# Kernel tuning notes

Hardware: AMD Instinct MI355X
Metric: run time of the kernel (lower is better)

Reference implementation:

```python
import jax, jax.numpy as jnp
import numpy as np
import jax.scipy.linalg as jsl


def _rbf(X1, X2, log_lengthscale):
    # squared-exponential kernel: exp(-0.5 * ||x1 - x2||^2 / ls^2)
    ls2 = jnp.exp(2.0 * log_lengthscale)
    d2 = (jnp.sum(X1 * X1, axis=1)[:, None]
          + jnp.sum(X2 * X2, axis=1)[None, :]
          - 2.0 * (X1 @ X2.T))
    return jnp.exp(-0.5 * jnp.maximum(d2, 0.0) / ls2)


def setup_inputs() -> dict:
    key = jax.random.key(0)
    k1, k2, k3, k4, k5 = jax.random.split(key, 5)
    N, D, l, rank, N_ = 1024, 8, 4, 2, 1024
    return {
        "X": jax.random.normal(k1, (N, D), dtype=jnp.float32),
        "test_X": jax.random.normal(k2, (N_, D), dtype=jnp.float32),
        "Y": jax.random.normal(k3, (N, l), dtype=jnp.float32),
        "log_noise": jnp.zeros((l,), dtype=jnp.float32),
        "covar_factor": jax.random.normal(k4, (l, rank), dtype=jnp.float32),
        "log_var": jax.random.normal(k5, (l,), dtype=jnp.float32),
        "log_lengthscale": jnp.zeros((), dtype=jnp.float32),
    }


def reference(X, test_X, Y, log_noise, covar_factor, log_var, log_lengthscale):
    N, l = Y.shape
    N_ = test_X.shape[0]
    # IndexKernel: B B^T + diag(exp(log_var))   -> (l, l)
    task_K = covar_factor @ covar_factor.T + jnp.diag(jnp.exp(log_var))
    # per-task noise kron identity -> (N*l, N*l)
    noise = jnp.kron(jnp.diag(jnp.exp(log_noise)), jnp.eye(N, dtype=X.dtype))
    # full Kronecker covariance and its Cholesky factor
    K = jnp.kron(task_K, _rbf(X, X, log_lengthscale)) + noise
    L = jnp.linalg.cholesky(K)                       # (N*l, N*l), lower
    Kx = jnp.kron(task_K, _rbf(X, test_X, log_lengthscale))     # (N*l, N_*l)
    Kxx = jnp.kron(task_K, _rbf(test_X, test_X, log_lengthscale))  # (N_*l, N_*l)
    A = jsl.solve_triangular(L, Kx, lower=True)      # L A = Kx
    Y_vec = Y.T.reshape(-1, 1)                        # vec of Y^T, (N*l, 1)
    V = jsl.solve_triangular(L, Y_vec, lower=True)
    fmean = A.T @ V                                   # (N_*l, 1)
    fvar = Kxx - A.T @ A                              # (N_*l, N_*l)
    return fmean, fvar, noise, fmean.reshape(l, N_).T
```

## Files before the change

### kernel.cpp

```cpp
#include <hip/hip_runtime.h>
#include <math.h>

#define NN 1024
#define NM (NN*NN)
#define NB 64
#define NBLK 16
#define NW 1152
#define BIG 4096

#define OFF_FVAR  ((size_t)4096)
#define OFF_NOISE ((size_t)(4096 + 16777216))
#define OFF_M4    ((size_t)(4096 + 2*16777216))

#define CPAD(c) ((c) + (((c)>>5)<<2))
#define WSTRIDE 140

struct GPParams {
  float tk[16];
  float E[16];
  float G[16];
  float lam[4];
};

__global__ void k_prep(const float* __restrict__ logn, const float* __restrict__ cf,
                       const float* __restrict__ logv, GPParams* __restrict__ P)
{
  if (threadIdx.x != 0 || blockIdx.x != 0) return;
  double tk[4][4], Dn[4], T[4][4], U[4][4];
  for (int a=0;a<4;a++) for (int b=0;b<4;b++){
    double s = 0.0;
    for (int r=0;r<2;r++) s += (double)cf[a*2+r]*(double)cf[b*2+r];
    if (a==b) s += exp((double)logv[a]);
    tk[a][b] = s;
  }
  for (int a=0;a<4;a++) Dn[a] = exp((double)logn[a]);
  for (int a=0;a<4;a++) for (int b=0;b<4;b++)
    T[a][b] = tk[a][b]/sqrt(Dn[a]*Dn[b]);
  for (int a=0;a<4;a++) for (int b=0;b<4;b++) U[a][b] = (a==b)?1.0:0.0;
  for (int sweep=0; sweep<40; sweep++){
    for (int p=0;p<3;p++) for (int q=p+1;q<4;q++){
      double apq = T[p][q];
      if (fabs(apq) < 1e-300) continue;
      double tau = (T[q][q]-T[p][p])/(2.0*apq);
      double t = (tau >= 0.0) ? 1.0/(tau + sqrt(1.0+tau*tau))
                              : 1.0/(tau - sqrt(1.0+tau*tau));
      double c = 1.0/sqrt(1.0+t*t), s = t*c;
      for (int k=0;k<4;k++){ double akp=T[k][p], akq=T[k][q];
        T[k][p]=c*akp - s*akq; T[k][q]=s*akp + c*akq; }
      for (int k=0;k<4;k++){ double apk=T[p][k], aqk=T[q][k];
        T[p][k]=c*apk - s*aqk; T[q][k]=s*apk + c*aqk; }
      for (int k=0;k<4;k++){ double ukp=U[k][p], ukq=U[k][q];
        U[k][p]=c*ukp - s*ukq; U[k][q]=s*ukp + c*ukq; }
    }
  }
  double E[4][4], G[4][4];
  for (int a=0;a<4;a++) for (int i=0;i<4;i++) E[a][i] = U[a][i]/sqrt(Dn[a]);
  for (int a=0;a<4;a++) for (int i=0;i<4;i++){
    double s=0; for (int b=0;b<4;b++) s += tk[a][b]*E[b][i];
    G[a][i]=s;
  }
  for (int a=0;a<4;a++) for (int b=0;b<4;b++){
    P->tk[a*4+b] = (float)tk[a][b];
    P->E [a*4+b] = (float)E[a][b];
    P->G [a*4+b] = (float)G[a][b];
  }
  for (int i=0;i<4;i++){
    double l = T[i][i];
    P->lam[i] = (float)(l > 0.0 ? l : 0.0);
  }
}

__global__ void k_rbf(const float* __restrict__ X1, const float* __restrict__ X2,
                      const float* __restrict__ logls, float* __restrict__ out)
{
  __shared__ float x1s[16][8];
  __shared__ float x2s[16][8];
  int tx = threadIdx.x, ty = threadIdx.y;
  int tid = ty*16 + tx;
  if (tid < 128){
    int r = tid>>3, d = tid&7;
    x1s[r][d] = X1[((size_t)blockIdx.y*16 + r)*8 + d];
  } else {
    int t2 = tid-128, r = t2>>3, d = t2&7;
    x2s[r][d] = X2[((size_t)blockIdx.x*16 + r)*8 + d];
  }
  __syncthreads();
  float ls2 = expf(2.0f*logls[0]);
  float d2 = 0.f;
  #pragma unroll
  for (int d=0; d<8; d++){ float df = x1s[ty][d]-x2s[tx][d]; d2 += df*df; }
  int i = blockIdx.y*16+ty, j = blockIdx.x*16+tx;
  out[(size_t)i*NN + j] = expf(-0.5f*d2/ls2);
}

__global__ void k_rbfM(const float* __restrict__ X1, const float* __restrict__ logls,
                       const GPParams* __restrict__ P, float* __restrict__ M)
{
  __shared__ float x1s[16][8];
  __shared__ float x2s[16][8];
  int tx = threadIdx.x, ty = threadIdx.y;
  int tid = ty*16 + tx;
  if (tid < 128){
    int r = tid>>3, d = tid&7;
    x1s[r][d] = X1[((size_t)blockIdx.y*16 + r)*8 + d];
  } else {
    int t2 = tid-128, r = t2>>3, d = t2&7;
    x2s[r][d] = X1[((size_t)blockIdx.x*16 + r)*8 + d];
  }
  __syncthreads();
  float ls2 = expf(2.0f*logls[0]);
  float d2 = 0.f;
  #pragma unroll
  for (int d=0; d<8; d++){ float df = x1s[ty][d]-x2s[tx][d]; d2 += df*df; }
  int i = blockIdx.y*16+ty, j = blockIdx.x*16+tx;
  float v = expf(-0.5f*d2/ls2);
  float diag = (i==j) ? 1.f : 0.f;
  size_t idx = (size_t)i*NN + j;
  #pragma unroll
  for (int z=0;z<4;z++)
    M[(size_t)z*NM + idx] = P->lam[z]*v + diag;
}

__global__ void k_uvec(const float* __restrict__ Y, const GPParams* __restrict__ P,
                       float* __restrict__ u)
{
  int n = blockIdx.x*256 + threadIdx.x;
  float y0 = Y[n*4+0], y1 = Y[n*4+1], y2 = Y[n*4+2], y3 = Y[n*4+3];
  #pragma unroll
  for (int i=0;i<4;i++)
    u[i*NN + n] = P->E[0*4+i]*y0 + P->E[1*4+i]*y1 + P->E[2*4+i]*y2 + P->E[3*4+i]*y3;
}

__device__ __forceinline__ void gemm64(const float* __restrict__ A, const float* __restrict__ B,
                                       float acc[4][4], int r0, int c0, bool sub)
{
  for (int p=0;p<64;p++){
    float ar[4], bc[4];
    #pragma unroll
    for (int ii=0;ii<4;ii++) ar[ii]=A[(r0+ii)*65+p];
    #pragma unroll
    for (int jj=0;jj<4;jj++) bc[jj]=B[p*65+c0+jj];
    if (sub){
      #pragma unroll
      for (int ii=0;ii<4;ii++)
        #pragma unroll
        for (int jj=0;jj<4;jj++) acc[ii][jj] -= ar[ii]*bc[jj];
    } else {
      #pragma unroll
      for (int ii=0;ii<4;ii++)
        #pragma unroll
        for (int jj=0;jj<4;jj++) acc[ii][jj] += ar[ii]*bc[jj];
    }
  }
}
__device__ __forceinline__ void gemm64T(const float* __restrict__ A, const float* __restrict__ B,
                                        float acc[4][4], int r0, int c0)
{
  for (int p=0;p<64;p++){
    float ar[4], bc[4];
    #pragma unroll
    for (int ii=0;ii<4;ii++) ar[ii]=A[(r0+ii)*65+p];
    #pragma unroll
    for (int jj=0;jj<4;jj++) bc[jj]=B[(c0+jj)*65+p];
    #pragma unroll
    for (int ii=0;ii<4;ii++)
      #pragma unroll
      for (int jj=0;jj<4;jj++) acc[ii][jj] += ar[ii]*bc[jj];
  }
}

__device__ __forceinline__ void inv_lower64(const float* __restrict__ L,
                                            float* __restrict__ inv,
                                            float* __restrict__ tmp, int tid)
{
  for (int idx=tid; idx<4160; idx+=256) inv[idx]=0.f;
  __syncthreads();
  if (tid < 64){
    int b = tid>>3, c = tid&7, base=b*8;
    for (int r=c;r<8;r++){
      float s = (r==c)?1.f:0.f;
      for (int j=c;j<r;j++) s -= L[(base+r)*65 + base+j]*inv[(base+j)*65 + base+c];
      inv[(base+r)*65 + base+c] = s / L[(base+r)*65 + base+r];
    }
  }
  __syncthreads();
  for (int bs=8; bs<=32; bs<<=1){
    int npair = 32/bs;
    int nout = npair*bs*bs;
    for (int idx=tid; idx<nout; idx+=256){
      int p0 = idx/(bs*bs), rem = idx%(bs*bs);
      int r = rem/bs, c = rem%bs, base = p0*2*bs;
      float s=0.f;
      for (int j=c;j<bs;j++)
        s += L[(base+bs+r)*65 + base+j]*inv[(base+j)*65 + base+c];
      tmp[idx]=s;
    }
    __syncthreads();
    for (int idx=tid; idx<nout; idx+=256){
      int p0 = idx/(bs*bs), rem = idx%(bs*bs);
      int r = rem/bs, c = rem%bs, base = p0*2*bs;
      float s=0.f;
      for (int j=0;j<=r;j++)
        s += inv[(base+bs+r)*65 + base+bs+j]*tmp[p0*bs*bs + j*bs + c];
      inv[(base+bs+r)*65 + base+c] = -s;
    }
    __syncthreads();
  }
}

__global__ __launch_bounds__(256) void k_potf2(float* __restrict__ M, float* __restrict__ Linv,
                                               float* __restrict__ Gbuf, int k)
{
  int z = blockIdx.x, tid = threadIdx.x;
  __shared__ float a[64*65];
  __shared__ float lo[64*65];
  __shared__ float tmp[1024];
  float* Mz = M + (size_t)z*NM;
  int base = k*NB;
  for (int idx=tid; idx<4096; idx+=256){
    int r=idx>>6, c=idx&63;
    a[r*65+c] = Mz[(size_t)(base+r)*NN + base + c];
  }
  int r = tid & 63, q = tid >> 6;
  for (int j=0;j<64;j++){
    __syncthreads();
    float d = a[j*65+j];
    float invd = 1.f/d;
    float rs = rsqrtf(d);
    if (q==0){
      if (r == j) lo[j*65+j] = sqrtf(d);
      else if (r > j) lo[r*65+j] = a[r*65+j]*rs;
      else lo[r*65+j] = 0.f;
    }
    if (r > j){
      float lrj = a[r*65+j]*invd;
      for (int c=j+1+q; c<=r; c+=4)
        a[r*65+c] -= lrj * a[c*65+j];
    }
  }
  __syncthreads();
  inv_lower64(lo, a, tmp, tid);
  float* Lg = Linv + ((size_t)z*NBLK + k)*(NB*NB);
  float* Td = Mz + (size_t)base*NN + base;
  for (int idx=tid; idx<4096; idx+=256){
    int rr=idx>>6, c=idx&63;
    float v = a[rr*65+c];
    Lg[rr*64+c] = v;
    Td[(size_t)rr*NN + c] = v;
  }
  {
    int r0=(tid>>4)*4, c0=(tid&15)*4;
    float g[4][4]={};
    for (int p=0;p<64;p++){
      float ar[4], bc[4];
      #pragma unroll
      for (int ii=0;ii<4;ii++) ar[ii]=a[p*65+r0+ii];
      #pragma unroll
      for (int jj=0;jj<4;jj++) bc[jj]=a[p*65+c0+jj];
      #pragma unroll
      for (int ii=0;ii<4;ii++)
        #pragma unroll
        for (int jj=0;jj<4;jj++) g[ii][jj]+=ar[ii]*bc[jj];
    }
    float* Gg = Gbuf + ((size_t)z*NBLK + k)*4096;
    #pragma unroll
    for (int ii=0;ii<4;ii++)
      *(float4*)&Gg[(r0+ii)*64 + c0] = make_float4(g[ii][0],g[ii][1],g[ii][2],g[ii][3]);
  }
}

__global__ __launch_bounds__(256) void k_csf(float* __restrict__ M, float* __restrict__ Linv,
                                             float* __restrict__ Gbuf, float* __restrict__ Lbuf, int k)
{
  int z = blockIdx.z;
  int tt = blockIdx.x, i2 = 0;
  while (tt >= i2+1){ tt -= (i2+1); i2++; }
  int bi = k+1+i2, bj = k+1+tt;
  bool fblk = (i2==0);
  __shared__ float pa[64*65];
  __shared__ float pb[64*65];
  __shared__ float li[64*65];
  float* Mz = M + (size_t)z*NM;
  float* Lb = Lbuf + (size_t)z*NM;
  int tid = threadIdx.x;
  int ty = tid>>4, tx = tid&15;
  int r0 = ty*4, c0 = tx*4;

  if (fblk){
    const float* Lg = Linv + ((size_t)z*NBLK + k)*(NB*NB);
    for (int idx=tid; idx<4096; idx+=256){
      int r=idx>>6, c=idx&63;
      li[r*65+c] = Lg[idx];
      pa[r*65+c] = Mz[(size_t)(bi*64+r)*NN + k*64 + c];
      pb[r*65+c] = Mz[(size_t)(bi*64+r)*NN + bi*64 + c];
    }
    __syncthreads();
    float sc[4][4]={};
    gemm64T(pa, li, sc, r0, c0);
    #pragma unroll
    for (int ii=0;ii<4;ii++)
      *(float4*)&Lb[(size_t)(bi*64+r0+ii)*NN + k*64+c0] =
        make_float4(sc[ii][0],sc[ii][1],sc[ii][2],sc[ii][3]);
    __syncthreads();
    #pragma unroll
    for (int ii=0;ii<4;ii++)
      #pragma unroll
      for (int jj=0;jj<4;jj++) pa[(r0+ii)*65+c0+jj] = sc[ii][jj];
    __syncthreads();
    float upd[4][4]={};
    gemm64T(pa, pa, upd, r0, c0);
    #pragma unroll
    for (int ii=0;ii<4;ii++)
      #pragma unroll
      for (int jj=0;jj<4;jj++) pb[(r0+ii)*65+c0+jj] -= upd[ii][jj];
    int r = tid & 63, q = tid >> 6;
    for (int j=0;j<64;j++){
      __syncthreads();
      float d = pb[j*65+j];
      float invd = 1.f/d;
      float rs = rsqrtf(d);
      if (q==0){
        if (r == j) li[j*65+j] = sqrtf(d);
        else if (r > j) li[r*65+j] = pb[r*65+j]*rs;
        else li[r*65+j] = 0.f;
      }
      if (r > j){
        float lrj = pb[r*65+j]*invd;
        for (int c=j+1+q; c<=r; c+=4)
          pb[r*65+c] -= lrj * pb[c*65+j];
      }
    }
    __syncthreads();
    inv_lower64(li, pa, pb, tid);
    float* Lg2 = Linv + ((size_t)z*NBLK + (k+1))*(NB*NB);
    float* Td  = Mz + (size_t)(bi*64)*NN + bi*64;
    for (int idx=tid; idx<4096; idx+=256){
      int rr=idx>>6, c=idx&63;
      float v = pa[rr*65+c];
      Lg2[rr*64+c] = v;
      Td[(size_t)rr*NN + c] = v;
    }
    {
      float g[4][4]={};
      for (int p=0;p<64;p++){
        float ar[4], bc[4];
        #pragma unroll
        for (int ii=0;ii<4;ii++) ar[ii]=pa[p*65+r0+ii];
        #pragma unroll
        for (int jj=0;jj<4;jj++) bc[jj]=pa[p*65+c0+jj];
        #pragma unroll
        for (int ii=0;ii<4;ii++)
          #pragma unroll
          for (int jj=0;jj<4;jj++) g[ii][jj]+=ar[ii]*bc[jj];
      }
      float* Gg = Gbuf + ((size_t)z*NBLK + (k+1))*4096;
      #pragma unroll
      for (int ii=0;ii<4;ii++)
        *(float4*)&Gg[(r0+ii)*64 + c0] = make_float4(g[ii][0],g[ii][1],g[ii][2],g[ii][3]);
    }
    return;
  }

  const float* Gg = Gbuf + ((size_t)z*NBLK + k)*4096;
  for (int idx=tid; idx<4096; idx+=256){
    int r=idx>>6, c=idx&63;
    li[r*65+c] = Gg[idx];
    pa[r*65+c] = Mz[(size_t)(bi*64+r)*NN + k*64 + c];
    pb[r*65+c] = Mz[(size_t)(bj*64+r)*NN + k*64 + c];
  }
  __syncthreads();
  float t[4][4]={};
  gemm64(pa, li, t, r0, c0, false);
  __syncthreads();
  #pragma unroll
  for (int ii=0;ii<4;ii++)
    #pragma unroll
    for (int jj=0;jj<4;jj++) li[(r0+ii)*65+c0+jj] = t[ii][jj];
  __syncthreads();
  float upd[4][4]={};
  gemm64T(li, pb, upd, r0, c0);
  #pragma unroll
  for (int ii=0;ii<4;ii++){
    float4* ptr = (float4*)&Mz[(size_t)(bi*64+r0+ii)*NN + bj*64+c0];
    float4 v = *ptr;
    v.x-=upd[ii][0]; v.y-=upd[ii][1]; v.z-=upd[ii][2]; v.w-=upd[ii][3];
    *ptr = v;
  }
  if (bj == k+1){
    __syncthreads();
    const float* Lg = Linv + ((size_t)z*NBLK + k)*(NB*NB);
    for (int idx=tid; idx<4096; idx+=256){
      int r=idx>>6, c=idx&63;
      pb[r*65+c] = Lg[idx];
    }
    __syncthreads();
    float sc[4][4]={};
    gemm64T(pa, pb, sc, r0, c0);
    #pragma unroll
    for (int ii=0;ii<4;ii++)
      *(float4*)&Lb[(size_t)(bi*64+r0+ii)*NN + k*64+c0] =
        make_float4(sc[ii][0],sc[ii][1],sc[ii][2],sc[ii][3]);
  }
}

__global__ __launch_bounds__(256) void k_dbl1(const float* __restrict__ Lbuf,
                                              const float* __restrict__ Linv,
                                              float* __restrict__ Tinv)
{
  int pair = blockIdx.x, z = blockIdx.y, tid = threadIdx.x;
  int b0 = 2*pair, b1 = 2*pair+1;
  __shared__ float l21[64*65];
  __shared__ float ai[64*65];
  __shared__ float tt[64*65];
  const float* Lb = Lbuf + (size_t)z*NM;
  const float* La = Linv + ((size_t)z*NBLK + b0)*(NB*NB);
  const float* Lc = Linv + ((size_t)z*NBLK + b1)*(NB*NB);
  for (int idx=tid; idx<4096; idx+=256){
    int r=idx>>6, c=idx&63;
    l21[r*65+c] = Lb[(size_t)(b1*64+r)*NN + b0*64 + c];
    ai[r*65+c]  = La[idx];
  }
  __syncthreads();
  int ty=tid>>4, tx=tid&15, r0=ty*4, c0=tx*4;
  float acc[4][4]={};
  gemm64(l21, ai, acc, r0, c0, false);
  __syncthreads();
  #pragma unroll
  for (int ii=0;ii<4;ii++)
    #pragma unroll
    for (int jj=0;jj<4;jj++) tt[(r0+ii)*65 + c0+jj] = acc[ii][jj];
  for (int idx=tid; idx<4096; idx+=256){
    int r=idx>>6, c=idx&63;
    ai[r*65+c] = Lc[idx];
  }
  __syncthreads();
  float fin[4][4]={};
  gemm64(ai, tt, fin, r0, c0, false);
  float* Tz = Tinv + (size_t)z*NM;
  #pragma unroll
  for (int ii=0;ii<4;ii++){
    float4 v = make_float4(-fin[ii][0],-fin[ii][1],-fin[ii][2],-fin[ii][3]);
    *(float4*)&Tz[(size_t)(b1*64+r0+ii)*NN + b0*64+c0] = v;
  }
}

__global__ __launch_bounds__(256) void k_dblT(const float* __restrict__ Lbuf,
                                              const float* __restrict__ Tinv,
                                              float* __restrict__ tb, int g64)
{
  int z = blockIdx.y, tid = threadIdx.x;
  int tpp = g64*g64;
  int pair = blockIdx.x / tpp;
  int tt2 = blockIdx.x % tpp;
  int ti = tt2 / g64, tj = tt2 % g64;
  int b0 = 2*pair*g64, b1 = b0 + g64;
  const float* Lb = Lbuf + (size_t)z*NM;
  const float* Tz = Tinv + (size_t)z*NM;
  __shared__ float lt[64*65];
  __shared__ float rt[64*65];
  int ty=tid>>4, tx=tid&15, r0=ty*4, c0=tx*4;
  float acc[4][4]={};
  for (int kb=tj; kb<g64; kb++){
    for (int idx=tid; idx<4096; idx+=256){
      int r=idx>>6, c=idx&63;
      lt[r*65+c] = Lb[(size_t)((b1+ti)*64+r)*NN + (b0+kb)*64 + c];
      rt[r*65+c] = Tz[(size_t)((b0+kb)*64+r)*NN + (b0+tj)*64 + c];
    }
    __syncthreads();
    gemm64(lt, rt, acc, r0, c0, false);
    __syncthreads();
  }
  int g = g64*64;
  float* tz = tb + (size_t)z*262144 + (size_t)pair*g*g;
  #pragma unroll
  for (int ii=0;ii<4;ii++){
    float4 v = make_float4(acc[ii][0],acc[ii][1],acc[ii][2],acc[ii][3]);
    *(float4*)&tz[(size_t)(ti*64+r0+ii)*g + tj*64+c0] = v;
  }
}

__global__ __launch_bounds__(256) void k_dblC(const float* __restrict__ tb,
                                              float* __restrict__ Tinv, int g64)
{
  int z = blockIdx.y, tid = threadIdx.x;
  int tpp = g64*g64;
  int pair = blockIdx.x / tpp;
  int tt2 = blockIdx.x % tpp;
  int ti = tt2 / g64, tj = tt2 % g64;
  int b0 = 2*pair*g64, b1 = b0 + g64;
  float* Tz = Tinv + (size_t)z*NM;
  int g = g64*64;
  const float* tz = tb + (size_t)z*262144 + (size_t)pair*g*g;
  __shared__ float lt[64*65];
  __shared__ float rt[64*65];
  int ty=tid>>4, tx=tid&15, r0=ty*4, c0=tx*4;
  float acc[4][4]={};
  for (int kb=0; kb<=ti; kb++){
    for (int idx=tid; idx<4096; idx+=256){
      int r=idx>>6, c=idx&63;
      lt[r*65+c] = Tz[(size_t)((b1+ti)*64+r)*NN + (b1+kb)*64 + c];
      rt[r*65+c] = tz[(size_t)(kb*64+r)*g + tj*64 + c];
    }
    __syncthreads();
    gemm64(lt, rt, acc, r0, c0, false);
    __syncthreads();
  }
  #pragma unroll
  for (int ii=0;ii<4;ii++){
    float4 v = make_float4(-acc[ii][0],-acc[ii][1],-acc[ii][2],-acc[ii][3]);
    *(float4*)&Tz[(size_t)((b1+ti)*64+r0+ii)*NN + b0*64+tj*64+c0] = v;
  }
}

__global__ __launch_bounds__(256) void k_wgemm(const float* __restrict__ Tinv,
                                               const float* __restrict__ R,
                                               const float* __restrict__ u,
                                               float* __restrict__ W)
{
  int ct = blockIdx.x;
  int bi = blockIdx.y;
  int z  = blockIdx.z;
  const float* Tz = Tinv + (size_t)z*NM;
  float* Wz = W + (size_t)z*NN*NW;
  __shared__ float At[64*68];
  __shared__ float Bs[64*132];
  int tid = threadIdx.x;
  int ty = tid>>4, tx = tid&15;
  float areg[16], breg[32];
  float acc[4][8] = {};
  #pragma unroll
  for (int i=0;i<16;i++){
    int idx=i*256+tid, r=idx>>6, c=idx&63;
    areg[i] = Tz[(size_t)(bi*64+r)*NN + c];
  }
  #pragma unroll
  for (int i=0;i<32;i++){
    int idx=i*256+tid, r=idx>>7, c=idx&127;
    breg[i] = (ct<8) ? R[(size_t)r*NN + ct*128 + c]
                     : ((c<4) ? u[c*NN + r] : 0.f);
  }
  for (int kb=0; kb<=bi; kb++){
    __syncthreads();
    #pragma unroll
    for (int i=0;i<16;i++){
      int idx=i*256+tid, r=idx>>6, c=idx&63;
      At[c*68 + r] = areg[i];
    }
    #pragma unroll
    for (int i=0;i<32;i++){
      int idx=i*256+tid, r=idx>>7, c=idx&127;
      Bs[r*132 + c] = breg[i];
    }
    if (kb < bi){
      int kn = kb+1;
      #pragma unroll
      for (int i=0;i<16;i++){
        int idx=i*256+tid, r=idx>>6, c=idx&63;
        areg[i] = Tz[(size_t)(bi*64+r)*NN + kn*64 + c];
      }
      #pragma unroll
      for (int i=0;i<32;i++){
        int idx=i*256+tid, r=idx>>7, c=idx&127;
        int gr = kn*64 + r;
        breg[i] = (ct<8) ? R[(size_t)gr*NN + ct*128 + c]
                         : ((c<4) ? u[c*NN + gr] : 0.f);
      }
    }
    __syncthreads();
    for (int p=0;p<64;p++){
      float4 a4 = *(const float4*)&At[p*68 + ty*4];
      float4 b0 = *(const float4*)&Bs[p*132 + tx*8];
      float4 b1 = *(const float4*)&Bs[p*132 + tx*8 + 4];
      float ar[4]={a4.x,a4.y,a4.z,a4.w};
      float bc[8]={b0.x,b0.y,b0.z,b0.w,b1.x,b1.y,b1.z,b1.w};
      #pragma unroll
      for (int ii=0;ii<4;ii++)
        #pragma unroll
        for (int jj=0;jj<8;jj++) acc[ii][jj] += ar[ii]*bc[jj];
    }
  }
  #pragma unroll
  for (int ii=0;ii<4;ii++){
    size_t row = (size_t)(bi*64 + ty*4 + ii)*NW + ct*128 + tx*8;
    *(float4*)&Wz[row]   = make_float4(acc[ii][0],acc[ii][1],acc[ii][2],acc[ii][3]);
    *(float4*)&Wz[row+4] = make_float4(acc[ii][4],acc[ii][5],acc[ii][6],acc[ii][7]);
  }
}

__global__ __launch_bounds__(256) void k_WtW(const float* __restrict__ W,
                                             float* __restrict__ Qa, float* __restrict__ Qb)
{
  int z = blockIdx.z;
  int ks = blockIdx.x / 36;
  int tt = blockIdx.x % 36, mi = 0;
  while (tt >= mi+1){ tt -= (mi+1); mi++; }
  int mj = tt;
  const float* Wz = W + (size_t)z*NN*NW;
  float* Qz = (ks ? Qb : Qa) + (size_t)z*NM;
  int mi0 = mi*128, mj0 = mj*128;
  __shared__ float as[16*WSTRIDE];
  __shared__ float bs[16*WSTRIDE];
  int tid = threadIdx.x;
  int ty = tid>>4, tx = tid&15;
  float areg[8], breg[8];
  float acc[8][8] = {};
  int nbase = ks*512;
  #pragma unroll
  for (int i=0;i<8;i++){
    int idx=i*256+tid, r=idx>>7, c=idx&127;
    areg[i] = Wz[(size_t)(nbase+r)*NW + mi0 + c];
    breg[i] = Wz[(size_t)(nbase+r)*NW + mj0 + c];
  }
  int ca = CPAD(ty*8), cb = CPAD(tx*8);
  for (int s=0;s<32;s++){
    __syncthreads();
    #pragma unroll
    for (int i=0;i<8;i++){
      int idx=i*256+tid, r=idx>>7, c=idx&127;
      as[r*WSTRIDE+CPAD(c)]=areg[i];
      bs[r*WSTRIDE+CPAD(c)]=breg[i];
    }
    if (s<31){
      int n0 = nbase + (s+1)*16;
      #pragma unroll
      for (int i=0;i<8;i++){
        int idx=i*256+tid, r=idx>>7, c=idx&127;
        areg[i] = Wz[(size_t)(n0+r)*NW + mi0 + c];
        breg[i] = Wz[(size_t)(n0+r)*NW + mj0 + c];
      }
    }
    __syncthreads();
    #pragma unroll
    for (int p=0;p<16;p++){
      float4 a0 = *(const float4*)&as[p*WSTRIDE + ca];
      float4 a1 = *(const float4*)&as[p*WSTRIDE + ca + 4];
      float4 b0 = *(const float4*)&bs[p*WSTRIDE + cb];
      float4 b1 = *(const float4*)&bs[p*WSTRIDE + cb + 4];
      float arf[8]={a0.x,a0.y,a0.z,a0.w,a1.x,a1.y,a1.z,a1.w};
      float bcf[8]={b0.x,b0.y,b0.z,b0.w,b1.x,b1.y,b1.z,b1.w};
      #pragma unroll
      for (int ii=0;ii<8;ii++)
        #pragma unroll
        for (int jj=0;jj<8;jj++) acc[ii][jj]+=arf[ii]*bcf[jj];
    }
  }
  for (int ii=0;ii<8;ii++){
    size_t row = (size_t)(mi0 + ty*8 + ii)*NN + mj0 + tx*8;
    *(float4*)&Qz[row]   = make_float4(acc[ii][0],acc[ii][1],acc[ii][2],acc[ii][3]);
    *(float4*)&Qz[row+4] = make_float4(acc[ii][4],acc[ii][5],acc[ii][6],acc[ii][7]);
  }
  if (mi != mj){
    for (int jj=0;jj<8;jj++){
      size_t row = (size_t)(mj0 + tx*8 + jj)*NN + mi0 + ty*8;
      *(float4*)&Qz[row]   = make_float4(acc[0][jj],acc[1][jj],acc[2][jj],acc[3][jj]);
      *(float4*)&Qz[row+4] = make_float4(acc[4][jj],acc[5][jj],acc[6][jj],acc[7][jj]);
    }
  }
}

__global__ void k_colmul(const float* __restrict__ W, float* __restrict__ wpart)
{
  int mc = blockIdx.x, z = blockIdx.y, ns = blockIdx.z, tid = threadIdx.x;
  __shared__ float ufs[256];
  const float* Wz = W + (size_t)z*NN*NW;
  ufs[tid] = Wz[(size_t)(ns*256+tid)*NW + 1024 + z];
  __syncthreads();
  int m = mc*256 + tid;
  float acc = 0.f;
  for (int n=0;n<256;n++)
    acc += Wz[(size_t)(ns*256+n)*NW + m]*ufs[n];
  wpart[(size_t)(z*4+ns)*1024 + m] = acc;
}

__global__ void k_fmeanout(const float* __restrict__ wpart, const GPParams* __restrict__ P,
                           float* __restrict__ out)
{
  int m = blockIdx.x*256 + threadIdx.x;
  float w[4];
  #pragma unroll
  for (int i=0;i<4;i++){
    float s=0.f;
    #pragma unroll
    for (int ns=0;ns<4;ns++) s += wpart[(size_t)(i*4+ns)*1024 + m];
    w[i]=s;
  }
  #pragma unroll
  for (int a=0;a<4;a++){
    float fm = 0.f;
    #pragma unroll
    for (int i=0;i<4;i++) fm += P->G[a*4+i]*w[i];
    out[a*NN + m] = fm;
    out[OFF_M4 + (size_t)m*4 + a] = fm;
  }
}

__global__ void k_fvar(const float* __restrict__ S, const float* __restrict__ Qa,
                       const float* __restrict__ Qb, const GPParams* __restrict__ P,
                       float* __restrict__ out)
{
  size_t idx = (size_t)blockIdx.x*256 + threadIdx.x;
  int m = (int)(idx>>10), mp = (int)(idx & 1023);
  float s = S[idx];
  float q[4];
  #pragma unroll
  for (int i=0;i<4;i++) q[i] = Qa[(size_t)i*NM + idx] + Qb[(size_t)i*NM + idx];
  float* fv = out + OFF_FVAR;
  #pragma unroll
  for (int a=0;a<4;a++)
    #pragma unroll
    for (int b=0;b<4;b++){
      float val = P->tk[a*4+b]*s;
      #pragma unroll
      for (int i=0;i<4;i++) val -= P->G[a*4+i]*P->G[b*4+i]*q[i];
      fv[(size_t)(a*NN+m)*BIG + (size_t)b*NN + mp] = val;
    }
}

__global__ void k_noise(const float* __restrict__ logn, float* __restrict__ out)
{
  size_t idx = (size_t)blockIdx.x*256 + threadIdx.x;
  int row = (int)(idx>>12), col = (int)(idx & 4095);
  out[OFF_NOISE + idx] = (row==col) ? expf(logn[row>>10]) : 0.f;
}

extern "C" void kernel_launch(void* const* d_in, const int* in_sizes, int n_in,
                              void* d_out, int out_size, void* d_ws, size_t ws_size,
                              hipStream_t stream)
{
  const float* X    = (const float*)d_in[0];
  const float* tX   = (const float*)d_in[1];
  const float* Y    = (const float*)d_in[2];
  const float* logn = (const float*)d_in[3];
  const float* cf   = (const float*)d_in[4];
  const float* logv = (const float*)d_in[5];
  const float* logls= (const float*)d_in[6];
  float* out = (float*)d_out;

  size_t need_floats = 64 + 4096 + 16384
                     + 2*(size_t)NM + 4*(size_t)NM + 262144 + 262144 + 4*(size_t)NM
                     + 4*(size_t)NN*NW;
  float* base;
  if (ws_size >= (need_floats + 1024)*sizeof(float)) base = (float*)d_ws;
  else base = out + OFF_NOISE;

  GPParams* P  = (GPParams*)base;
  float* u     = base + 64;
  float* wpart = u + 4096;
  float* R     = wpart + 16384;
  float* S     = R + NM;
  float* M     = S + NM;
  float* Linv  = M + 4*(size_t)NM;
  float* Gbuf  = Linv + 262144;
  float* Lbuf  = Gbuf + 262144;
  float* W     = Lbuf + 4*(size_t)NM;
  float* Tinv  = M;
  float* Qa    = M;
  float* Qb    = Lbuf;
  float* tb    = W;

  dim3 b16(16,16);

  k_prep<<<1, 1, 0, stream>>>(logn, cf, logv, P);
  k_rbf <<<dim3(64,64), b16, 0, stream>>>(X,  tX, logls, R);
  k_rbf <<<dim3(64,64), b16, 0, stream>>>(tX, tX, logls, S);
  k_rbfM<<<dim3(64,64), b16, 0, stream>>>(X, logls, P, M);
  k_uvec<<<dim3(4), 256, 0, stream>>>(Y, P, u);

  k_potf2<<<dim3(4), 256, 0, stream>>>(M, Linv, Gbuf, 0);
  for (int k=0;k<NBLK-1;k++){
    int nb = NBLK-1-k;
    k_csf<<<dim3(nb*(nb+1)/2, 1, 4), 256, 0, stream>>>(M, Linv, Gbuf, Lbuf, k);
  }

  k_dbl1<<<dim3(8,4), 256, 0, stream>>>(Lbuf, Linv, Tinv);
  for (int g64=2; g64<=8; g64*=2){
    int np = 8/g64;
    k_dblT<<<dim3(np*g64*g64, 4), 256, 0, stream>>>(Lbuf, Tinv, tb, g64);
    k_dblC<<<dim3(np*g64*g64, 4), 256, 0, stream>>>(tb, Tinv, g64);
  }

  k_wgemm<<<dim3(9,16,4), 256, 0, stream>>>(Tinv, R, u, W);

  k_WtW<<<dim3(72,1,4), 256, 0, stream>>>(W, Qa, Qb);

  k_colmul<<<dim3(4,4,4), 256, 0, stream>>>(W, wpart);
  k_fmeanout<<<dim3(4), 256, 0, stream>>>(wpart, P, out);
  k_fvar<<<dim3(NM/256), 256, 0, stream>>>(S, Qa, Qb, P, out);
  k_noise<<<dim3(16777216/256), 256, 0, stream>>>(logn, out);
}
```

Baseline: 1.966 ms.

## Fuse Cholesky, inversion and W-GEMM into one cooperative persistent kernel

Replaces the long chain of small launches (potf2, 15 csf steps, the doubling inversion stages, wgemm) with one cooperative kernel of 256 blocks that loops over tiles and uses grid-wide syncs between stages, cutting launch and tail gaps. If the cooperative launch fails it falls back to the original per-stage kernels. It also splits the WtW reduction into three K-slices instead of two for more parallelism, and moves the W buffer into the fvar output region to free workspace. Grid syncs and persistent tile loops may leave blocks idle at stages with few tiles.

```diff
diff --git a/kernel.cpp b/kernel.cpp
--- a/kernel.cpp
+++ b/kernel.cpp
@@ -1,5 +1,8 @@
 #include <hip/hip_runtime.h>
+#include <hip/hip_cooperative_groups.h>
 #include <math.h>
+
+namespace cg = cooperative_groups;
 
 #define NN 1024
 #define NM (NN*NN)
@@ -132,7 +135,7 @@
 }
 
 __device__ __forceinline__ void gemm64(const float* __restrict__ A, const float* __restrict__ B,
-                                       float acc[4][4], int r0, int c0, bool sub)
+                                       float acc[4][4], int r0, int c0)
 {
   for (int p=0;p<64;p++){
     float ar[4], bc[4];
@@ -140,17 +143,10 @@
     for (int ii=0;ii<4;ii++) ar[ii]=A[(r0+ii)*65+p];
     #pragma unroll
     for (int jj=0;jj<4;jj++) bc[jj]=B[p*65+c0+jj];
-    if (sub){
-      #pragma unroll
-      for (int ii=0;ii<4;ii++)
-        #pragma unroll
-        for (int jj=0;jj<4;jj++) acc[ii][jj] -= ar[ii]*bc[jj];
-    } else {
-      #pragma unroll
-      for (int ii=0;ii<4;ii++)
-        #pragma unroll
-        for (int jj=0;jj<4;jj++) acc[ii][jj] += ar[ii]*bc[jj];
-    }
+    #pragma unroll
+    for (int ii=0;ii<4;ii++)
+      #pragma unroll
+      for (int jj=0;jj<4;jj++) acc[ii][jj] += ar[ii]*bc[jj];
   }
 }
 __device__ __forceinline__ void gemm64T(const float* __restrict__ A, const float* __restrict__ B,
@@ -208,15 +204,12 @@
   }
 }
 
-__global__ __launch_bounds__(256) void k_potf2(float* __restrict__ M, float* __restrict__ Linv,
-                                               float* __restrict__ Gbuf, int k)
-{
-  int z = blockIdx.x, tid = threadIdx.x;
-  __shared__ float a[64*65];
-  __shared__ float lo[64*65];
-  __shared__ float tmp[1024];
+__device__ void potf2_body(float* M, float* Linv, float* Gbuf, int k, int z, int tid,
+                           float* a, float* lo, float* tmp)
+{
   float* Mz = M + (size_t)z*NM;
   int base = k*NB;
+  __syncthreads();
   for (int idx=tid; idx<4096; idx+=256){
     int r=idx>>6, c=idx&63;
     a[r*65+c] = Mz[(size_t)(base+r)*NN + base + c];
@@ -269,22 +262,19 @@
   }
 }
 
-__global__ __launch_bounds__(256) void k_csf(float* __restrict__ M, float* __restrict__ Linv,
-                                             float* __restrict__ Gbuf, float* __restrict__ Lbuf, int k)
-{
-  int z = blockIdx.z;
-  int tt = blockIdx.x, i2 = 0;
+__device__ void csf_tile_body(float* M, float* Linv, float* Gbuf, float* Lbuf,
+                              int k, int z, int tt, int tid,
+                              float* pa, float* pb, float* li)
+{
+  int i2 = 0;
   while (tt >= i2+1){ tt -= (i2+1); i2++; }
   int bi = k+1+i2, bj = k+1+tt;
   bool fblk = (i2==0);
-  __shared__ float pa[64*65];
-  __shared__ float pb[64*65];
-  __shared__ float li[64*65];
   float* Mz = M + (size_t)z*NM;
   float* Lb = Lbuf + (size_t)z*NM;
-  int tid = threadIdx.x;
   int ty = tid>>4, tx = tid&15;
   int r0 = ty*4, c0 = tx*4;
+  __syncthreads();
 
   if (fblk){
     const float* Lg = Linv + ((size_t)z*NBLK + k)*(NB*NB);
@@ -358,63 +348,58 @@
       for (int ii=0;ii<4;ii++)
         *(float4*)&Gg[(r0+ii)*64 + c0] = make_float4(g[ii][0],g[ii][1],g[ii][2],g[ii][3]);
     }
-    return;
-  }
-
-  const float* Gg = Gbuf + ((size_t)z*NBLK + k)*4096;
-  for (int idx=tid; idx<4096; idx+=256){
-    int r=idx>>6, c=idx&63;
-    li[r*65+c] = Gg[idx];
-    pa[r*65+c] = Mz[(size_t)(bi*64+r)*NN + k*64 + c];
-    pb[r*65+c] = Mz[(size_t)(bj*64+r)*NN + k*64 + c];
-  }
-  __syncthreads();
-  float t[4][4]={};
-  gemm64(pa, li, t, r0, c0, false);
-  __syncthreads();
-  #pragma unroll
-  for (int ii=0;ii<4;ii++)
-    #pragma unroll
-    for (int jj=0;jj<4;jj++) li[(r0+ii)*65+c0+jj] = t[ii][jj];
-  __syncthreads();
-  float upd[4][4]={};
-  gemm64T(li, pb, upd, r0, c0);
-  #pragma unroll
-  for (int ii=0;ii<4;ii++){
-    float4* ptr = (float4*)&Mz[(size_t)(bi*64+r0+ii)*NN + bj*64+c0];
-    float4 v = *ptr;
-    v.x-=upd[ii][0]; v.y-=upd[ii][1]; v.z-=upd[ii][2]; v.w-=upd[ii][3];
-    *ptr = v;
-  }
-  if (bj == k+1){
-    __syncthreads();
-    const float* Lg = Linv + ((size_t)z*NBLK + k)*(NB*NB);
+  } else {
+    const float* Gg = Gbuf + ((size_t)z*NBLK + k)*4096;
     for (int idx=tid; idx<4096; idx+=256){
       int r=idx>>6, c=idx&63;
-      pb[r*65+c] = Lg[idx];
-    }
-    __syncthreads();
-    float sc[4][4]={};
-    gemm64T(pa, pb, sc, r0, c0);
+      li[r*65+c] = Gg[idx];
+      pa[r*65+c] = Mz[(size_t)(bi*64+r)*NN + k*64 + c];
+      pb[r*65+c] = Mz[(size_t)(bj*64+r)*NN + k*64 + c];
+    }
+    __syncthreads();
+    float t[4][4]={};
+    gemm64(pa, li, t, r0, c0);
+    __syncthreads();
     #pragma unroll
     for (int ii=0;ii<4;ii++)
-      *(float4*)&Lb[(size_t)(bi*64+r0+ii)*NN + k*64+c0] =
-        make_float4(sc[ii][0],sc[ii][1],sc[ii][2],sc[ii][3]);
-  }
-}
-
-__global__ __launch_bounds__(256) void k_dbl1(const float* __restrict__ Lbuf,
-                                              const float* __restrict__ Linv,
-                                              float* __restrict__ Tinv)
-{
-  int pair = blockIdx.x, z = blockIdx.y, tid = threadIdx.x;
+      #pragma unroll
+      for (int jj=0;jj<4;jj++) li[(r0+ii)*65+c0+jj] = t[ii][jj];
+    __syncthreads();
+    float upd[4][4]={};
+    gemm64T(li, pb, upd, r0, c0);
+    #pragma unroll
+    for (int ii=0;ii<4;ii++){
+      float4* ptr = (float4*)&Mz[(size_t)(bi*64+r0+ii)*NN + bj*64+c0];
+      float4 v = *ptr;
+      v.x-=upd[ii][0]; v.y-=upd[ii][1]; v.z-=upd[ii][2]; v.w-=upd[ii][3];
+      *ptr = v;
+    }
+    if (bj == k+1){
+      __syncthreads();
+      const float* Lg = Linv + ((size_t)z*NBLK + k)*(NB*NB);
+      for (int idx=tid; idx<4096; idx+=256){
+        int r=idx>>6, c=idx&63;
+        pb[r*65+c] = Lg[idx];
+      }
+      __syncthreads();
+      float sc[4][4]={};
+      gemm64T(pa, pb, sc, r0, c0);
+      #pragma unroll
+      for (int ii=0;ii<4;ii++)
+        *(float4*)&Lb[(size_t)(bi*64+r0+ii)*NN + k*64+c0] =
+          make_float4(sc[ii][0],sc[ii][1],sc[ii][2],sc[ii][3]);
+    }
+  }
+}
+
+__device__ void dbl1_body(const float* Lbuf, const float* Linv, float* Tinv,
+                          int pair, int z, int tid, float* l21, float* ai, float* tt)
+{
   int b0 = 2*pair, b1 = 2*pair+1;
-  __shared__ float l21[64*65];
-  __shared__ float ai[64*65];
-  __shared__ float tt[64*65];
   const float* Lb = Lbuf + (size_t)z*NM;
   const float* La = Linv + ((size_t)z*NBLK + b0)*(NB*NB);
   const float* Lc = Linv + ((size_t)z*NBLK + b1)*(NB*NB);
+  __syncthreads();
   for (int idx=tid; idx<4096; idx+=256){
     int r=idx>>6, c=idx&63;
     l21[r*65+c] = Lb[(size_t)(b1*64+r)*NN + b0*64 + c];
@@ -423,7 +408,7 @@
   __syncthreads();
   int ty=tid>>4, tx=tid&15, r0=ty*4, c0=tx*4;
   float acc[4][4]={};
-  gemm64(l21, ai, acc, r0, c0, false);
+  gemm64(l21, ai, acc, r0, c0);
   __syncthreads();
   #pragma unroll
   for (int ii=0;ii<4;ii++)
@@ -435,7 +420,7 @@
   }
   __syncthreads();
   float fin[4][4]={};
-  gemm64(ai, tt, fin, r0, c0, false);
+  gemm64(ai, tt, fin, r0, c0);
   float* Tz = Tinv + (size_t)z*NM;
   #pragma unroll
   for (int ii=0;ii<4;ii++){
@@ -444,22 +429,19 @@
   }
 }
 
-__global__ __launch_bounds__(256) void k_dblT(const float* __restrict__ Lbuf,
-                                              const float* __restrict__ Tinv,
-                                              float* __restrict__ tb, int g64)
-{
-  int z = blockIdx.y, tid = threadIdx.x;
+__device__ void dblT_body(const float* Lbuf, const float* Tinv, float* tb,
+                          int g64, int rr, int z, int tid, float* lt, float* rt)
+{
   int tpp = g64*g64;
-  int pair = blockIdx.x / tpp;
-  int tt2 = blockIdx.x % tpp;
+  int pair = rr / tpp;
+  int tt2 = rr % tpp;
   int ti = tt2 / g64, tj = tt2 % g64;
   int b0 = 2*pair*g64, b1 = b0 + g64;
   const float* Lb = Lbuf + (size_t)z*NM;
   const float* Tz = Tinv + (size_t)z*NM;
-  __shared__ float lt[64*65];
-  __shared__ float rt[64*65];
   int ty=tid>>4, tx=tid&15, r0=ty*4, c0=tx*4;
   float acc[4][4]={};
+  __syncthreads();
   for (int kb=tj; kb<g64; kb++){
     for (int idx=tid; idx<4096; idx+=256){
       int r=idx>>6, c=idx&63;
@@ -467,7 +449,7 @@
       rt[r*65+c] = Tz[(size_t)((b0+kb)*64+r)*NN + (b0+tj)*64 + c];
     }
     __syncthreads();
-    gemm64(lt, rt, acc, r0, c0, false);
+    gemm64(lt, rt, acc, r0, c0);
     __syncthreads();
   }
   int g = g64*64;
@@ -479,22 +461,20 @@
   }
 }
 
-__global__ __launch_bounds__(256) void k_dblC(const float* __restrict__ tb,
-                                              float* __restrict__ Tinv, int g64)
-{
-  int z = blockIdx.y, tid = threadIdx.x;
+__device__ void dblC_body(const float* tb, float* Tinv,
+                          int g64, int rr, int z, int tid, float* lt, float* rt)
+{
   int tpp = g64*g64;
-  int pair = blockIdx.x / tpp;
-  int tt2 = blockIdx.x % tpp;
+  int pair = rr / tpp;
+  int tt2 = rr % tpp;
   int ti = tt2 / g64, tj = tt2 % g64;
   int b0 = 2*pair*g64, b1 = b0 + g64;
   float* Tz = Tinv + (size_t)z*NM;
   int g = g64*64;
   const float* tz = tb + (size_t)z*262144 + (size_t)pair*g*g;
-  __shared__ float lt[64*65];
-  __shared__ float rt[64*65];
   int ty=tid>>4, tx=tid&15, r0=ty*4, c0=tx*4;
   float acc[4][4]={};
+  __syncthreads();
   for (int kb=0; kb<=ti; kb++){
     for (int idx=tid; idx<4096; idx+=256){
       int r=idx>>6, c=idx&63;
@@ -502,7 +482,7 @@
       rt[r*65+c] = tz[(size_t)(kb*64+r)*g + tj*64 + c];
     }
     __syncthreads();
-    gemm64(lt, rt, acc, r0, c0, false);
+    gemm64(lt, rt, acc, r0, c0);
     __syncthreads();
   }
   #pragma unroll
@@ -512,22 +492,17 @@
   }
 }
 
-__global__ __launch_bounds__(256) void k_wgemm(const float* __restrict__ Tinv,
-                                               const float* __restrict__ R,
-                                               const float* __restrict__ u,
-                                               float* __restrict__ W)
-{
-  int ct = blockIdx.x;
-  int bi = blockIdx.y;
-  int z  = blockIdx.z;
+__device__ void wgemm_body(const float* Tinv, const float* R, const float* u, float* W,
+                           int ct, int bi, int z, int tid, float* lds)
+{
+  float* At = lds;
+  float* Bs = lds + 4352;
   const float* Tz = Tinv + (size_t)z*NM;
   float* Wz = W + (size_t)z*NN*NW;
-  __shared__ float At[64*68];
-  __shared__ float Bs[64*132];
-  int tid = threadIdx.x;
   int ty = tid>>4, tx = tid&15;
   float areg[16], breg[32];
   float acc[4][8] = {};
+  __syncthreads();
   #pragma unroll
   for (int i=0;i<16;i++){
     int idx=i*256+tid, r=idx>>6, c=idx&63;
@@ -587,8 +562,97 @@
   }
 }
 
+__global__ __launch_bounds__(256) void k_mega(float* M, float* Linv, float* Gbuf, float* Lbuf,
+                                              float* tb, float* R, float* u, float* W)
+{
+  cg::grid_group gg = cg::this_grid();
+  __shared__ float lds[12800];
+  float* pa = lds;
+  float* pb = lds + 4160;
+  float* li = lds + 8320;
+  int tid = threadIdx.x;
+
+  if (blockIdx.x < 4)
+    potf2_body(M, Linv, Gbuf, 0, blockIdx.x, tid, pa, pb, li);
+  gg.sync();
+
+  for (int k=0;k<15;k++){
+    int nb = 15-k;
+    int tpz = nb*(nb+1)/2;
+    int ntile = tpz*4;
+    for (int t = blockIdx.x; t < ntile; t += gridDim.x){
+      int z = t / tpz;
+      int tt = t % tpz;
+      csf_tile_body(M, Linv, Gbuf, Lbuf, k, z, tt, tid, pa, pb, li);
+    }
+    gg.sync();
+  }
+
+  if (blockIdx.x < 32){
+    int pair = blockIdx.x & 7, z = blockIdx.x >> 3;
+    dbl1_body(Lbuf, Linv, M, pair, z, tid, pa, pb, li);
+  }
+  gg.sync();
+
+  for (int g64=2; g64<=8; g64*=2){
+    int np = 8/g64, tpp = g64*g64;
+    int per_z = np*tpp;
+    int ntile = per_z*4;
+    for (int t = blockIdx.x; t < ntile; t += gridDim.x){
+      int z = t / per_z, rr = t % per_z;
+      dblT_body(Lbuf, M, tb, g64, rr, z, tid, pa, pb);
+    }
+    gg.sync();
+    for (int t = blockIdx.x; t < ntile; t += gridDim.x){
+      int z = t / per_z, rr = t % per_z;
+      dblC_body(tb, M, g64, rr, z, tid, pa, pb);
+    }
+    gg.sync();
+  }
+
+  for (int t = blockIdx.x; t < 576; t += gridDim.x){
+    int z = t / 144, rem = t % 144;
+    int bi = rem / 9, ct = rem % 9;
+    wgemm_body(M, R, u, W, ct, bi, z, tid, lds);
+  }
+}
+
+__global__ __launch_bounds__(256) void kw_potf2(float* M, float* Linv, float* Gbuf, int k)
+{
+  __shared__ float lds[12800];
+  potf2_body(M, Linv, Gbuf, k, blockIdx.x, threadIdx.x, lds, lds+4160, lds+8320);
+}
+__global__ __launch_bounds__(256) void kw_csf(float* M, float* Linv, float* Gbuf, float* Lbuf, int k)
+{
+  __shared__ float lds[12800];
+  csf_tile_body(M, Linv, Gbuf, Lbuf, k, blockIdx.z, blockIdx.x, threadIdx.x,
+                lds, lds+4160, lds+8320);
+}
+__global__ __launch_bounds__(256) void kw_dbl1(const float* Lbuf, const float* Linv, float* Tinv)
+{
+  __shared__ float lds[12800];
+  dbl1_body(Lbuf, Linv, Tinv, blockIdx.x, blockIdx.y, threadIdx.x, lds, lds+4160, lds+8320);
+}
+__global__ __launch_bounds__(256) void kw_dblT(const float* Lbuf, const float* Tinv, float* tb, int g64)
+{
+  __shared__ float lds[8320];
+  dblT_body(Lbuf, Tinv, tb, g64, blockIdx.x, blockIdx.y, threadIdx.x, lds, lds+4160);
+}
+__global__ __launch_bounds__(256) void kw_dblC(const float* tb, float* Tinv, int g64)
+{
+  __shared__ float lds[8320];
+  dblC_body(tb, Tinv, g64, blockIdx.x, blockIdx.y, threadIdx.x, lds, lds+4160);
+}
+__global__ __launch_bounds__(256) void kw_wgemm(const float* Tinv, const float* R,
+                                                const float* u, float* W)
+{
+  __shared__ float lds[12800];
+  wgemm_body(Tinv, R, u, W, blockIdx.x, blockIdx.y, blockIdx.z, threadIdx.x, lds);
+}
+
 __global__ __launch_bounds__(256) void k_WtW(const float* __restrict__ W,
-                                             float* __restrict__ Qa, float* __restrict__ Qb)
+                                             float* __restrict__ Qa, float* __restrict__ Qb,
+                                             float* __restrict__ Qc)
 {
   int z = blockIdx.z;
   int ks = blockIdx.x / 36;
@@ -596,7 +660,7 @@
   while (tt >= mi+1){ tt -= (mi+1); mi++; }
   int mj = tt;
   const float* Wz = W + (size_t)z*NN*NW;
-  float* Qz = (ks ? Qb : Qa) + (size_t)z*NM;
+  float* Qz = (ks==0 ? Qa : (ks==1 ? Qb : Qc)) + (size_t)z*NM;
   int mi0 = mi*128, mj0 = mj*128;
   __shared__ float as[16*WSTRIDE];
   __shared__ float bs[16*WSTRIDE];
@@ -604,7 +668,8 @@
   int ty = tid>>4, tx = tid&15;
   float areg[8], breg[8];
   float acc[8][8] = {};
-  int nbase = ks*512;
+  int nbase = ks*352;
+  int nsteps = (ks==2)?20:22;
   #pragma unroll
   for (int i=0;i<8;i++){
     int idx=i*256+tid, r=idx>>7, c=idx&127;
@@ -612,7 +677,7 @@
     breg[i] = Wz[(size_t)(nbase+r)*NW + mj0 + c];
   }
   int ca = CPAD(ty*8), cb = CPAD(tx*8);
-  for (int s=0;s<32;s++){
+  for (int s=0;s<nsteps;s++){
     __syncthreads();
     #pragma unroll
     for (int i=0;i<8;i++){
@@ -620,7 +685,7 @@
       as[r*WSTRIDE+CPAD(c)]=areg[i];
       bs[r*WSTRIDE+CPAD(c)]=breg[i];
     }
-    if (s<31){
+    if (s<nsteps-1){
       int n0 = nbase + (s+1)*16;
       #pragma unroll
       for (int i=0;i<8;i++){
@@ -695,15 +760,16 @@
 }
 
 __global__ void k_fvar(const float* __restrict__ S, const float* __restrict__ Qa,
-                       const float* __restrict__ Qb, const GPParams* __restrict__ P,
-                       float* __restrict__ out)
+                       const float* __restrict__ Qb, const float* __restrict__ Qc,
+                       const GPParams* __restrict__ P, float* __restrict__ out)
 {
   size_t idx = (size_t)blockIdx.x*256 + threadIdx.x;
   int m = (int)(idx>>10), mp = (int)(idx & 1023);
   float s = S[idx];
   float q[4];
   #pragma unroll
-  for (int i=0;i<4;i++) q[i] = Qa[(size_t)i*NM + idx] + Qb[(size_t)i*NM + idx];
+  for (int i=0;i<4;i++)
+    q[i] = Qa[(size_t)i*NM + idx] + Qb[(size_t)i*NM + idx] + Qc[(size_t)i*NM + idx];
   float* fv = out + OFF_FVAR;
   #pragma unroll
   for (int a=0;a<4;a++)
@@ -737,8 +803,8 @@
   float* out = (float*)d_out;
 
   size_t need_floats = 64 + 4096 + 16384
-                     + 2*(size_t)NM + 4*(size_t)NM + 262144 + 262144 + 4*(size_t)NM
-                     + 4*(size_t)NN*NW;
+                     + 2*(size_t)NM + 4*(size_t)NM + 262144 + 262144
+                     + 4*(size_t)NM + 4*(size_t)NM;
   float* base;
   if (ws_size >= (need_floats + 1024)*sizeof(float)) base = (float*)d_ws;
   else base = out + OFF_NOISE;
@@ -751,12 +817,13 @@
   float* M     = S + NM;
   float* Linv  = M + 4*(size_t)NM;
   float* Gbuf  = Linv + 262144;
-  float* Lbuf  = Gbuf + 262144;
-  float* W     = Lbuf + 4*(size_t)NM;
-  float* Tinv  = M;
+  float* TQ    = Gbuf + 262144;
+  float* Lbuf  = TQ + 4*(size_t)NM;
+  float* W     = out + OFF_FVAR;
   float* Qa    = M;
   float* Qb    = Lbuf;
-  float* tb    = W;
+  float* Qc    = TQ;
+  float* tb    = TQ;
 
   dim3 b16(16,16);
 
@@ -766,25 +833,33 @@
   k_rbfM<<<dim3(64,64), b16, 0, stream>>>(X, logls, P, M);
   k_uvec<<<dim3(4), 256, 0, stream>>>(Y, P, u);
 
-  k_potf2<<<dim3(4), 256, 0, stream>>>(M, Linv, Gbuf, 0);
-  for (int k=0;k<NBLK-1;k++){
-    int nb = NBLK-1-k;
-    k_csf<<<dim3(nb*(nb+1)/2, 1, 4), 256, 0, stream>>>(M, Linv, Gbuf, Lbuf, k);
-  }
-
-  k_dbl1<<<dim3(8,4), 256, 0, stream>>>(Lbuf, Linv, Tinv);
-  for (int g64=2; g64<=8; g64*=2){
-    int np = 8/g64;
-    k_dblT<<<dim3(np*g64*g64, 4), 256, 0, stream>>>(Lbuf, Tinv, tb, g64);
-    k_dblC<<<dim3(np*g64*g64, 4), 256, 0, stream>>>(tb, Tinv, g64);
-  }
-
-  k_wgemm<<<dim3(9,16,4), 256, 0, stream>>>(Tinv, R, u, W);
-
-  k_WtW<<<dim3(72,1,4), 256, 0, stream>>>(W, Qa, Qb);
+  hipError_t ce;
+  {
+    void* kargs[] = { (void*)&M, (void*)&Linv, (void*)&Gbuf, (void*)&Lbuf,
+                      (void*)&tb, (void*)&R, (void*)&u, (void*)&W };
+    ce = hipLaunchCooperativeKernel((const void*)k_mega, dim3(256), dim3(256),
+                                    kargs, 0, stream);
+  }
+  if (ce != hipSuccess){
+    (void)hipGetLastError();
+    kw_potf2<<<dim3(4), 256, 0, stream>>>(M, Linv, Gbuf, 0);
+    for (int k=0;k<15;k++){
+      int nb = 15-k;
+      kw_csf<<<dim3(nb*(nb+1)/2, 1, 4), 256, 0, stream>>>(M, Linv, Gbuf, Lbuf, k);
+    }
+    kw_dbl1<<<dim3(8,4), 256, 0, stream>>>(Lbuf, Linv, M);
+    for (int g64=2; g64<=8; g64*=2){
+      int np = 8/g64;
+      kw_dblT<<<dim3(np*g64*g64, 4), 256, 0, stream>>>(Lbuf, M, tb, g64);
+      kw_dblC<<<dim3(np*g64*g64, 4), 256, 0, stream>>>(tb, M, g64);
+    }
+    kw_wgemm<<<dim3(9,16,4), 256, 0, stream>>>(M, R, u, W);
+  }
+
+  k_WtW<<<dim3(108,1,4), 256, 0, stream>>>(W, Qa, Qb, Qc);
 
   k_colmul<<<dim3(4,4,4), 256, 0, stream>>>(W, wpart);
   k_fmeanout<<<dim3(4), 256, 0, stream>>>(wpart, P, out);
-  k_fvar<<<dim3(NM/256), 256, 0, stream>>>(S, Qa, Qb, P, out);
+  k_fvar<<<dim3(NM/256), 256, 0, stream>>>(S, Qa, Qb, Qc, P, out);
   k_noise<<<dim3(16777216/256), 256, 0, stream>>>(logn, out);
 }
```

Result: slower. 2.591 ms (+31.8%).
